# Optimization experiments

Measured on AMD Instinct MI355X. Metric: run time of the kernel, lower is better.

The kernel has to match this reference:

```python
import jax, jax.numpy as jnp
import numpy as np

B, T, N, E = 8, 32, 128, 2048
IN_DIM, HID, OUT = 512, 512, 512
SLOPE = 0.2  # GATConv default negative_slope


def setup_inputs() -> dict:
    key = jax.random.key(0)
    ks = jax.random.split(key, 12)
    x = jax.random.normal(ks[0], (B, T, N, IN_DIM), jnp.float32)
    edge_index = jax.random.randint(ks[1], (B, T, 2, E), 0, N)
    valid_step_index = jax.random.randint(ks[2], (B,), 1, T + 1)
    def lin(k, o, i):
        return jax.random.normal(k, (o, i), jnp.float32) / np.sqrt(i).astype(np.float32)
    W1 = lin(ks[3], HID, IN_DIM)
    a1_src = jax.random.normal(ks[4], (HID,), jnp.float32) / np.sqrt(HID).astype(np.float32)
    a1_dst = jax.random.normal(ks[5], (HID,), jnp.float32) / np.sqrt(HID).astype(np.float32)
    b1 = jnp.zeros((HID,), jnp.float32)
    W2 = lin(ks[6], OUT, HID)
    a2_src = jax.random.normal(ks[7], (OUT,), jnp.float32) / np.sqrt(OUT).astype(np.float32)
    a2_dst = jax.random.normal(ks[8], (OUT,), jnp.float32) / np.sqrt(OUT).astype(np.float32)
    b2 = jnp.zeros((OUT,), jnp.float32)
    W_time = jax.random.normal(ks[9], (T, T), jnp.float32) / np.sqrt(T).astype(np.float32)
    b_time = jnp.zeros((T,), jnp.float32)
    return dict(x=x, edge_index=edge_index, valid_step_index=valid_step_index,
                W1=W1, a1_src=a1_src, a1_dst=a1_dst, b1=b1,
                W2=W2, a2_src=a2_src, a2_dst=a2_dst, b2=b2,
                W_time=W_time, b_time=b_time)


def _gat(x, src, dst, W, a_src, a_dst, b):
    # Single-head PyG GATConv (concat=True, heads=1), self-loops already appended.
    n = x.shape[0]
    h = x @ W.T                                             # [N, H]
    e = jax.nn.leaky_relu((h @ a_src)[src] + (h @ a_dst)[dst], SLOPE)  # [E]
    m = jax.ops.segment_max(e, dst, num_segments=n)
    m = jnp.where(jnp.isfinite(m), m, 0.0)
    p = jnp.exp(e - m[dst])
    denom = jax.ops.segment_sum(p, dst, num_segments=n)
    alpha = p / denom[dst]                                  # segment softmax over incoming edges
    return jax.ops.segment_sum(h[src] * alpha[:, None], dst, num_segments=n) + b


def reference(x, edge_index, valid_step_index, W1, a1_src, a1_dst, b1,
              W2, a2_src, a2_dst, b2, W_time, b_time):
    b_, t_, n_, _ = x.shape
    g = b_ * t_
    xf = x.reshape(g, n_, -1)
    ei = edge_index.reshape(g, 2, -1)
    # add self loops (PyG GATConv default add_self_loops=True)
    loops = jnp.broadcast_to(jnp.arange(n_)[None, None, :], (g, 2, n_))
    ei = jnp.concatenate([ei, loops], axis=-1)
    src, dst = ei[:, 0], ei[:, 1]
    gat = jax.vmap(_gat, in_axes=(0, 0, 0, None, None, None, None))
    h = jax.nn.gelu(gat(xf, src, dst, W1, a1_src, a1_dst, b1), approximate=False)
    # F.dropout(p=0.2) is identity in eval mode
    h = gat(h, src, dst, W2, a2_src, a2_dst, b2)
    y = h.reshape(b_, t_, n_, -1)
    mask = (jnp.arange(t_)[None, :] < valid_step_index[:, None]).astype(y.dtype)
    y = y * mask[:, :, None, None]
    # TemporalConv: Conv2d(T, T, 1) over time-as-channel = linear mix across time, then GELU, residual
    fused = jax.nn.gelu(jnp.einsum('ts,bsnf->btnf', W_time, y)
                        + b_time[None, :, None, None], approximate=False)
    return fused + y
```

## Files before the change

kernel.cpp:

```cpp
#include <hip/hip_runtime.h>

using u16 = unsigned short;
using u32 = unsigned int;

typedef __bf16 bf16x8 __attribute__((ext_vector_type(8)));
typedef float  f32x4  __attribute__((ext_vector_type(4)));

__device__ __forceinline__ u16 f2bf(float f) {
    u32 u = __float_as_uint(f);
    u32 r = u + 0x7fffu + ((u >> 16) & 1u);
    return (u16)(r >> 16);
}
__device__ __forceinline__ float gelu_f(float x) {
    return 0.5f * x * (1.0f + erff(x * 0.70710678118654752440f));
}

#define GLOAD16(gp, lp) __builtin_amdgcn_global_load_lds( \
    (const __attribute__((address_space(1))) void*)(gp),  \
    (__attribute__((address_space(3))) void*)(lp), 16, 0, 0)
#define WAITV4  asm volatile("s_waitcnt vmcnt(4)" ::: "memory")
#define WAITV0  asm volatile("s_waitcnt vmcnt(0)" ::: "memory")
#define WAITL0  asm volatile("s_waitcnt lgkmcnt(0)" ::: "memory")

__global__ __launch_bounds__(256) void prep_kernel(
    const float* __restrict__ x, const float* __restrict__ W1, const float* __restrict__ W2,
    u16* __restrict__ Xb, u16* __restrict__ W1b, u16* __restrict__ W2b,
    float* __restrict__ Z)
{
    const int i0 = blockIdx.x * 256 + threadIdx.x;
    const int stride = gridDim.x * 256;
    if (i0 < 32768) ((float4*)Z)[i0] = make_float4(0.f, 0.f, 0.f, 0.f);
    for (int i = i0; i < 65536; i += stride) {
        float4 v = ((const float4*)W1)[i];
        ushort4 o; o.x = f2bf(v.x); o.y = f2bf(v.y); o.z = f2bf(v.z); o.w = f2bf(v.w);
        ((ushort4*)W1b)[i] = o;
    }
    for (int i = i0; i < 65536; i += stride) {
        float4 v = ((const float4*)W2)[i];
        ushort4 o; o.x = f2bf(v.x); o.y = f2bf(v.y); o.z = f2bf(v.z); o.w = f2bf(v.w);
        ((ushort4*)W2b)[i] = o;
    }
    for (int i = i0; i < 4194304; i += stride) {
        float4 v = ((const float4*)x)[i];
        ushort4 o; o.x = f2bf(v.x); o.y = f2bf(v.y); o.z = f2bf(v.z); o.w = f2bf(v.w);
        ((ushort4*)Xb)[i] = o;
    }
}

__global__ __launch_bounds__(256) void gat_gemm(
    const u16* __restrict__ A, const u16* __restrict__ Wb,
    const float* __restrict__ a_s, const float* __restrict__ a_d,
    u16* __restrict__ HT, float* __restrict__ SS, float* __restrict__ SD)
{
    __shared__ __align__(16) u16 As[2][128 * 32];
    __shared__ __align__(16) u16 Bs[2][128 * 32];
    __shared__ float sA[128], dA[128];

    const int tid  = threadIdx.x;
    const int lane = tid & 63;
    const int w    = tid >> 6;
    const int wm   = w & 1, wn = w >> 1;
    const int fr   = lane & 15;
    const int grp  = lane >> 4;
    const int bid  = (blockIdx.x & 7) * 128 + (blockIdx.x >> 3);
    const int g    = bid >> 2;
    const int tn   = (bid & 3) * 128;

    if (tid < 128) { sA[tid] = 0.f; dA[tid] = 0.f; }

    const int l3 = lane >> 3, l7 = lane & 7;
    const int cs = l7 ^ l3;
    const u16* Ag0 = A  + (size_t)g * 65536
                   + (size_t)(w * 32 + 2 * l3 + (cs >> 2)) * 512 + (cs & 3) * 8;
    const u16* Bg0 = Wb + (size_t)(tn + w * 32 + 2 * l3 + (cs >> 2)) * 512 + (cs & 3) * 8;

    const int sw = ((((fr & 1) << 2) | grp) ^ ((fr >> 1) & 7)) * 8;

    f32x4 acc[4][4] = {};

    GLOAD16(Ag0,                 &As[0][w * 1024]);
    GLOAD16(Ag0 + 16 * 512,      &As[0][w * 1024 + 512]);
    GLOAD16(Bg0,                 &Bs[0][w * 1024]);
    GLOAD16(Bg0 + 16 * 512,      &Bs[0][w * 1024 + 512]);
    GLOAD16(Ag0 + 32,            &As[1][w * 1024]);
    GLOAD16(Ag0 + 16 * 512 + 32, &As[1][w * 1024 + 512]);
    GLOAD16(Bg0 + 32,            &Bs[1][w * 1024]);
    GLOAD16(Bg0 + 16 * 512 + 32, &Bs[1][w * 1024 + 512]);

    for (int kt = 0; kt < 16; ++kt) {
        const int cur = kt & 1;
        if (kt < 15) { WAITV4; } else { WAITV0; }
        __builtin_amdgcn_s_barrier();
        bf16x8 af[4], bf[4];
        #pragma unroll
        for (int i = 0; i < 4; ++i) {
            af[i] = *(const bf16x8*)&As[cur][(wm * 32 + i * 8 + (fr >> 1)) * 64 + sw];
            bf[i] = *(const bf16x8*)&Bs[cur][(wn * 32 + i * 8 + (fr >> 1)) * 64 + sw];
        }
        WAITL0;
        __builtin_amdgcn_sched_barrier(0);
        __builtin_amdgcn_s_barrier();
        if (kt < 14) {
            GLOAD16(Ag0 + (kt + 2) * 32,            &As[cur][w * 1024]);
            GLOAD16(Ag0 + 16 * 512 + (kt + 2) * 32, &As[cur][w * 1024 + 512]);
            GLOAD16(Bg0 + (kt + 2) * 32,            &Bs[cur][w * 1024]);
            GLOAD16(Bg0 + 16 * 512 + (kt + 2) * 32, &Bs[cur][w * 1024 + 512]);
        }
        #pragma unroll
        for (int i = 0; i < 4; ++i)
            #pragma unroll
            for (int j = 0; j < 4; ++j)
                acc[i][j] = __builtin_amdgcn_mfma_f32_16x16x32_bf16(af[i], bf[j], acc[i][j], 0, 0, 0);
    }

    float asv[4], adv[4];
    #pragma unroll
    for (int j = 0; j < 4; ++j) {
        int f = tn + wn * 64 + j * 16 + fr;
        asv[j] = a_s[f]; adv[j] = a_d[f];
    }
    u16* Hg = HT + (size_t)g * 65536;
    #pragma unroll
    for (int i = 0; i < 4; ++i) {
        int node0 = wm * 64 + i * 16 + grp * 4;
        #pragma unroll
        for (int j = 0; j < 4; ++j) {
            int f = tn + wn * 64 + j * 16 + fr;
            ushort4 o;
            o.x = f2bf(acc[i][j][0]); o.y = f2bf(acc[i][j][1]);
            o.z = f2bf(acc[i][j][2]); o.w = f2bf(acc[i][j][3]);
            *(ushort4*)&Hg[(size_t)f * 128 + node0] = o;
        }
        #pragma unroll
        for (int r = 0; r < 4; ++r) {
            float s = acc[i][0][r] * asv[0] + acc[i][1][r] * asv[1]
                    + acc[i][2][r] * asv[2] + acc[i][3][r] * asv[3];
            float d = acc[i][0][r] * adv[0] + acc[i][1][r] * adv[1]
                    + acc[i][2][r] * adv[2] + acc[i][3][r] * adv[3];
            #pragma unroll
            for (int off = 1; off < 16; off <<= 1) {
                s += __shfl_xor(s, off);
                d += __shfl_xor(d, off);
            }
            if (fr == 0) {
                atomicAdd(&sA[node0 + r], s);
                atomicAdd(&dA[node0 + r], d);
            }
        }
    }
    __syncthreads();
    if (tid < 128) {
        atomicAdd(&SS[g * 128 + tid], sA[tid]);
        atomicAdd(&SD[g * 128 + tid], dA[tid]);
    }
}

template<int MODE>
__global__ __launch_bounds__(512) void gat_agg(
    const u16* __restrict__ HT, const int* __restrict__ ei,
    const float* __restrict__ SS, const float* __restrict__ SD,
    const float* __restrict__ bias, const int* __restrict__ valid,
    u16* __restrict__ outU, float* __restrict__ outF)
{
    __shared__ u16 Hts[32768];
    __shared__ u32 cntw[2048];
    __shared__ float stf[512];

    const int tid  = threadIdx.x;
    const int lane = tid & 63;
    const int w    = tid >> 6;
    const int rl   = lane & 15;
    const int grp  = lane >> 4;
    const int q    = blockIdx.x;
    const int g    = (q & 7) * 32 + (q >> 4);
    const int hf   = (q >> 3) & 1;
    const int bb   = g >> 5, tt = g & 31;

    const int4* es = (const int4*)(ei + (size_t)g * 4096);
    int4 e0 = es[tid], e1 = es[512 + tid];

    const u16* Hg = HT + (size_t)g * 65536 + (size_t)hf * 256 * 128;
    #pragma unroll
    for (int it = 0; it < 8; ++it) {
        int fl = it * 32 + (tid >> 4);
        int blk = tid & 15;
        GLOAD16(Hg + (size_t)fl * 128 + ((blk ^ (fl & 15)) * 8), &Hts[it * 4096 + w * 512]);
    }

    for (int i = tid; i < 2048; i += 512) cntw[i] = 0u;
    if (tid < 128) {
        stf[tid]       = SS[g * 128 + tid];
        stf[128 + tid] = SD[g * 128 + tid];
    }
    __syncthreads();

    atomicAdd(&cntw[e1.x * 16 + (e0.x >> 3)], 1u << ((e0.x & 7) * 4));
    atomicAdd(&cntw[e1.y * 16 + (e0.y >> 3)], 1u << ((e0.y & 7) * 4));
    atomicAdd(&cntw[e1.z * 16 + (e0.z >> 3)], 1u << ((e0.z & 7) * 4));
    atomicAdd(&cntw[e1.w * 16 + (e0.w >> 3)], 1u << ((e0.w & 7) * 4));
    if (tid < 128) atomicAdd(&cntw[tid * 16 + (tid >> 3)], 1u << ((tid & 7) * 4));
    __syncthreads();

    for (int r = 0; r < 16; ++r) {
        int m = w * 16 + r;
        float sdm = stf[128 + m];
        u32 w0 = cntw[m * 16 + (lane >> 3)];
        u32 w1 = cntw[m * 16 + 8 + (lane >> 3)];
        u32 c0 = (w0 >> ((lane & 7) * 4)) & 15u;
        u32 c1 = (w1 >> ((lane & 7) * 4)) & 15u;
        float E0 = stf[lane] + sdm;      E0 = E0 > 0.f ? E0 : 0.2f * E0;
        float E1 = stf[lane + 64] + sdm; E1 = E1 > 0.f ? E1 : 0.2f * E1;
        float mx = fmaxf(c0 ? E0 : -1e30f, c1 ? E1 : -1e30f);
        #pragma unroll
        for (int off = 1; off < 64; off <<= 1) mx = fmaxf(mx, __shfl_xor(mx, off));
        float p = (c0 ? (float)c0 * __expf(E0 - mx) : 0.f)
                + (c1 ? (float)c1 * __expf(E1 - mx) : 0.f);
        #pragma unroll
        for (int off = 1; off < 64; off <<= 1) p += __shfl_xor(p, off);
        if (lane == 0) { stf[256 + m] = mx; stf[384 + m] = 1.f / p; }
    }
    __syncthreads();

    const int m = w * 16 + rl;
    const float sdm = stf[128 + m], Mm = stf[256 + m], rDm = stf[384 + m];
    bf16x8 pa[4];
    #pragma unroll
    for (int kb = 0; kb < 4; ++kb) {
        u32 word = cntw[m * 16 + kb * 4 + grp];
        #pragma unroll
        for (int e = 0; e < 8; ++e) {
            u32 c = (word >> (e * 4)) & 15u;
            int s = kb * 32 + grp * 8 + e;
            float ev = stf[s] + sdm; ev = ev > 0.f ? ev : 0.2f * ev;
            float p = c ? (float)c * __expf(ev - Mm) * rDm : 0.f;
            pa[kb][e] = (__bf16)p;
        }
    }

    const float msk = (MODE == 1) ? ((tt < valid[bb]) ? 1.f : 0.f) : 1.f;
    #pragma unroll 1
    for (int jc = 0; jc < 4; ++jc) {
        f32x4 acc2[4] = {};
        __builtin_amdgcn_s_setprio(1);
        #pragma unroll
        for (int j4 = 0; j4 < 4; ++j4) {
            int fl = jc * 64 + j4 * 16 + rl;
            #pragma unroll
            for (int kb = 0; kb < 4; ++kb) {
                bf16x8 hb = *(const bf16x8*)&Hts[fl * 128 + (((kb * 4 + grp) ^ (fl & 15)) * 8)];
                acc2[j4] = __builtin_amdgcn_mfma_f32_16x16x32_bf16(pa[kb], hb, acc2[j4], 0, 0, 0);
            }
        }
        __builtin_amdgcn_s_setprio(0);
        #pragma unroll
        for (int j4 = 0; j4 < 4; ++j4) {
            int f = hf * 256 + jc * 64 + j4 * 16 + rl;
            float bv = bias[f];
            #pragma unroll
            for (int r = 0; r < 4; ++r) {
                int m2 = w * 16 + grp * 4 + r;
                if (MODE == 0)
                    outU[(size_t)g * 65536 + m2 * 512 + f] = f2bf(gelu_f(acc2[j4][r] + bv));
                else
                    outF[(size_t)g * 65536 + m2 * 512 + f] = (acc2[j4][r] + bv) * msk;
            }
        }
    }
}

__global__ __launch_bounds__(256) void timemix_kernel(float* __restrict__ y,
                                                      const float* __restrict__ Wt,
                                                      const float* __restrict__ bt) {
    __shared__ float wsm[1024];
    __shared__ float bts[32];
    int tid = threadIdx.x;
    for (int i = tid; i < 1024; i += 256) wsm[i] = Wt[i];
    if (tid < 32) bts[tid] = bt[tid];
    __syncthreads();
    int blk = blockIdx.x;
    int b = blk >> 8;
    int rem = blk & 255;
    int n = rem >> 1;
    int f = (rem & 1) * 256 + tid;
    size_t base = ((size_t)b * 4096 + n) * 512 + f;
    float ys[32];
    #pragma unroll
    for (int s = 0; s < 32; ++s) ys[s] = y[base + (size_t)s * 65536];
    #pragma unroll
    for (int t = 0; t < 32; ++t) {
        float a = bts[t];
        #pragma unroll
        for (int s = 0; s < 32; ++s) a += wsm[t * 32 + s] * ys[s];
        y[base + (size_t)t * 65536] = gelu_f(a) + ys[t];
    }
}

extern "C" void kernel_launch(void* const* d_in, const int* in_sizes, int n_in,
                              void* d_out, int out_size, void* d_ws, size_t ws_size,
                              hipStream_t stream) {
    const float* x     = (const float*)d_in[0];
    const int*   ei    = (const int*)d_in[1];
    const int*   valid = (const int*)d_in[2];
    const float* W1    = (const float*)d_in[3];
    const float* a1s   = (const float*)d_in[4];
    const float* a1d   = (const float*)d_in[5];
    const float* b1    = (const float*)d_in[6];
    const float* W2    = (const float*)d_in[7];
    const float* a2s   = (const float*)d_in[8];
    const float* a2d   = (const float*)d_in[9];
    const float* b2    = (const float*)d_in[10];
    const float* Wt    = (const float*)d_in[11];
    const float* bt    = (const float*)d_in[12];
    float* out = (float*)d_out;

    char* ws = (char*)d_ws;
    u16* Xb    = (u16*)(ws);
    u16* HTb   = (u16*)(ws + 33554432);
    u16* W1b   = (u16*)(ws + 67108864);
    u16* W2b   = (u16*)(ws + 67633152);
    float* SS1 = (float*)(ws + 68157440);
    float* SD1 = (float*)(ws + 68288512);
    float* SS2 = (float*)(ws + 68419584);
    float* SD2 = (float*)(ws + 68550656);

    prep_kernel<<<2048, 256, 0, stream>>>(x, W1, W2, Xb, W1b, W2b, SS1);

    gat_gemm<<<1024, 256, 0, stream>>>(Xb, W1b, a1s, a1d, HTb, SS1, SD1);
    gat_agg<0><<<512, 512, 0, stream>>>(HTb, ei, SS1, SD1, b1, nullptr, Xb, nullptr);

    gat_gemm<<<1024, 256, 0, stream>>>(Xb, W2b, a2s, a2d, HTb, SS2, SD2);
    gat_agg<1><<<512, 512, 0, stream>>>(HTb, ei, SS2, SD2, b2, valid, nullptr, out);

    timemix_kernel<<<2048, 256, 0, stream>>>(out, Wt, bt);
}
```

Before: 178.3 us.

## Fuse fp32-to-bf16 input conversion into first GAT GEMM A-tile loads

The first GEMM now reads fp32 x directly, converts it to bf16 in registers and writes the result to LDS with the swizzled layout. This removes the separate prep pass that wrote and reread a bf16 copy of x. The trade is a register-staged, single-barrier pipeline instead of the async global_load_lds double buffer. The aggregation kernel also swaps __syncthreads for explicit waitcnt plus s_barrier.

```diff
diff --git a/kernel.cpp b/kernel.cpp
--- a/kernel.cpp
+++ b/kernel.cpp
@@ -10,6 +10,9 @@
     u32 u = __float_as_uint(f);
     u32 r = u + 0x7fffu + ((u >> 16) & 1u);
     return (u16)(r >> 16);
+}
+__device__ __forceinline__ u32 pack2(float lo, float hi) {
+    return (u32)f2bf(lo) | ((u32)f2bf(hi) << 16);
 }
 __device__ __forceinline__ float gelu_f(float x) {
     return 0.5f * x * (1.0f + erff(x * 0.70710678118654752440f));
@@ -21,10 +24,11 @@
 #define WAITV4  asm volatile("s_waitcnt vmcnt(4)" ::: "memory")
 #define WAITV0  asm volatile("s_waitcnt vmcnt(0)" ::: "memory")
 #define WAITL0  asm volatile("s_waitcnt lgkmcnt(0)" ::: "memory")
+#define WAITVL0 asm volatile("s_waitcnt vmcnt(0) lgkmcnt(0)" ::: "memory")
 
 __global__ __launch_bounds__(256) void prep_kernel(
-    const float* __restrict__ x, const float* __restrict__ W1, const float* __restrict__ W2,
-    u16* __restrict__ Xb, u16* __restrict__ W1b, u16* __restrict__ W2b,
+    const float* __restrict__ W1, const float* __restrict__ W2,
+    u16* __restrict__ W1b, u16* __restrict__ W2b,
     float* __restrict__ Z)
 {
     const int i0 = blockIdx.x * 256 + threadIdx.x;
@@ -40,15 +44,11 @@
         ushort4 o; o.x = f2bf(v.x); o.y = f2bf(v.y); o.z = f2bf(v.z); o.w = f2bf(v.w);
         ((ushort4*)W2b)[i] = o;
     }
-    for (int i = i0; i < 4194304; i += stride) {
-        float4 v = ((const float4*)x)[i];
-        ushort4 o; o.x = f2bf(v.x); o.y = f2bf(v.y); o.z = f2bf(v.z); o.w = f2bf(v.w);
-        ((ushort4*)Xb)[i] = o;
-    }
-}
-
+}
+
+template<int AF32>
 __global__ __launch_bounds__(256) void gat_gemm(
-    const u16* __restrict__ A, const u16* __restrict__ Wb,
+    const void* __restrict__ Av, const u16* __restrict__ Wb,
     const float* __restrict__ a_s, const float* __restrict__ a_d,
     u16* __restrict__ HT, float* __restrict__ SS, float* __restrict__ SD)
 {
@@ -70,47 +70,111 @@
 
     const int l3 = lane >> 3, l7 = lane & 7;
     const int cs = l7 ^ l3;
-    const u16* Ag0 = A  + (size_t)g * 65536
-                   + (size_t)(w * 32 + 2 * l3 + (cs >> 2)) * 512 + (cs & 3) * 8;
     const u16* Bg0 = Wb + (size_t)(tn + w * 32 + 2 * l3 + (cs >> 2)) * 512 + (cs & 3) * 8;
 
     const int sw = ((((fr & 1) << 2) | grp) ^ ((fr >> 1) & 7)) * 8;
 
     f32x4 acc[4][4] = {};
 
-    GLOAD16(Ag0,                 &As[0][w * 1024]);
-    GLOAD16(Ag0 + 16 * 512,      &As[0][w * 1024 + 512]);
-    GLOAD16(Bg0,                 &Bs[0][w * 1024]);
-    GLOAD16(Bg0 + 16 * 512,      &Bs[0][w * 1024 + 512]);
-    GLOAD16(Ag0 + 32,            &As[1][w * 1024]);
-    GLOAD16(Ag0 + 16 * 512 + 32, &As[1][w * 1024 + 512]);
-    GLOAD16(Bg0 + 32,            &Bs[1][w * 1024]);
-    GLOAD16(Bg0 + 16 * 512 + 32, &Bs[1][w * 1024 + 512]);
-
-    for (int kt = 0; kt < 16; ++kt) {
-        const int cur = kt & 1;
-        if (kt < 15) { WAITV4; } else { WAITV0; }
-        __builtin_amdgcn_s_barrier();
-        bf16x8 af[4], bf[4];
-        #pragma unroll
-        for (int i = 0; i < 4; ++i) {
-            af[i] = *(const bf16x8*)&As[cur][(wm * 32 + i * 8 + (fr >> 1)) * 64 + sw];
-            bf[i] = *(const bf16x8*)&Bs[cur][(wn * 32 + i * 8 + (fr >> 1)) * 64 + sw];
-        }
-        WAITL0;
-        __builtin_amdgcn_sched_barrier(0);
-        __builtin_amdgcn_s_barrier();
-        if (kt < 14) {
-            GLOAD16(Ag0 + (kt + 2) * 32,            &As[cur][w * 1024]);
-            GLOAD16(Ag0 + 16 * 512 + (kt + 2) * 32, &As[cur][w * 1024 + 512]);
-            GLOAD16(Bg0 + (kt + 2) * 32,            &Bs[cur][w * 1024]);
-            GLOAD16(Bg0 + 16 * 512 + (kt + 2) * 32, &Bs[cur][w * 1024 + 512]);
-        }
-        #pragma unroll
-        for (int i = 0; i < 4; ++i)
-            #pragma unroll
-            for (int j = 0; j < 4; ++j)
-                acc[i][j] = __builtin_amdgcn_mfma_f32_16x16x32_bf16(af[i], bf[j], acc[i][j], 0, 0, 0);
+    if constexpr (AF32 == 0) {
+        const u16* Ag0 = (const u16*)Av + (size_t)g * 65536
+                       + (size_t)(w * 32 + 2 * l3 + (cs >> 2)) * 512 + (cs & 3) * 8;
+        GLOAD16(Ag0,                 &As[0][w * 1024]);
+        GLOAD16(Ag0 + 16 * 512,      &As[0][w * 1024 + 512]);
+        GLOAD16(Bg0,                 &Bs[0][w * 1024]);
+        GLOAD16(Bg0 + 16 * 512,      &Bs[0][w * 1024 + 512]);
+        GLOAD16(Ag0 + 32,            &As[1][w * 1024]);
+        GLOAD16(Ag0 + 16 * 512 + 32, &As[1][w * 1024 + 512]);
+        GLOAD16(Bg0 + 32,            &Bs[1][w * 1024]);
+        GLOAD16(Bg0 + 16 * 512 + 32, &Bs[1][w * 1024 + 512]);
+
+        for (int kt = 0; kt < 16; ++kt) {
+            const int cur = kt & 1;
+            if (kt < 15) { WAITV4; } else { WAITV0; }
+            __builtin_amdgcn_s_barrier();
+            bf16x8 af[4], bf[4];
+            #pragma unroll
+            for (int i = 0; i < 4; ++i) {
+                af[i] = *(const bf16x8*)&As[cur][(wm * 32 + i * 8 + (fr >> 1)) * 64 + sw];
+                bf[i] = *(const bf16x8*)&Bs[cur][(wn * 32 + i * 8 + (fr >> 1)) * 64 + sw];
+            }
+            WAITL0;
+            __builtin_amdgcn_sched_barrier(0);
+            __builtin_amdgcn_s_barrier();
+            if (kt < 14) {
+                GLOAD16(Ag0 + (kt + 2) * 32,            &As[cur][w * 1024]);
+                GLOAD16(Ag0 + 16 * 512 + (kt + 2) * 32, &As[cur][w * 1024 + 512]);
+                GLOAD16(Bg0 + (kt + 2) * 32,            &Bs[cur][w * 1024]);
+                GLOAD16(Bg0 + 16 * 512 + (kt + 2) * 32, &Bs[cur][w * 1024 + 512]);
+            }
+            #pragma unroll
+            for (int i = 0; i < 4; ++i)
+                #pragma unroll
+                for (int j = 0; j < 4; ++j)
+                    acc[i][j] = __builtin_amdgcn_mfma_f32_16x16x32_bf16(af[i], bf[j], acc[i][j], 0, 0, 0);
+        }
+    } else {
+        const float* xg = (const float*)Av + (size_t)g * 65536;
+        const int R  = tid >> 1;
+        const int cb = (tid & 1) * 2;
+        const float* xrow = xg + (size_t)R * 512 + cb * 8;
+        const int P  = R >> 1;
+        const int b0 = (((R & 1) << 2) | cb) ^ (P & 7);
+        const int b1 = (((R & 1) << 2) | (cb + 1)) ^ (P & 7);
+        const int wa0 = P * 64 + b0 * 8;
+        const int wa1 = P * 64 + b1 * 8;
+
+        {
+            f32x4 xa = *(const f32x4*)(xrow + 0);
+            f32x4 xb = *(const f32x4*)(xrow + 4);
+            f32x4 xc = *(const f32x4*)(xrow + 8);
+            f32x4 xd = *(const f32x4*)(xrow + 12);
+            uint4 q0, q1;
+            q0.x = pack2(xa[0], xa[1]); q0.y = pack2(xa[2], xa[3]);
+            q0.z = pack2(xb[0], xb[1]); q0.w = pack2(xb[2], xb[3]);
+            q1.x = pack2(xc[0], xc[1]); q1.y = pack2(xc[2], xc[3]);
+            q1.z = pack2(xd[0], xd[1]); q1.w = pack2(xd[2], xd[3]);
+            *(uint4*)&As[0][wa0] = q0;
+            *(uint4*)&As[0][wa1] = q1;
+            GLOAD16(Bg0,            &Bs[0][w * 1024]);
+            GLOAD16(Bg0 + 16 * 512, &Bs[0][w * 1024 + 512]);
+        }
+        __syncthreads();
+
+        for (int kt = 0; kt < 16; ++kt) {
+            const int cur = kt & 1, nb = cur ^ 1;
+            f32x4 xa, xb, xc, xd;
+            if (kt < 15) {
+                const float* xr = xrow + (kt + 1) * 32;
+                xa = *(const f32x4*)(xr + 0);
+                xb = *(const f32x4*)(xr + 4);
+                xc = *(const f32x4*)(xr + 8);
+                xd = *(const f32x4*)(xr + 12);
+                GLOAD16(Bg0 + (kt + 1) * 32,            &Bs[nb][w * 1024]);
+                GLOAD16(Bg0 + 16 * 512 + (kt + 1) * 32, &Bs[nb][w * 1024 + 512]);
+            }
+            bf16x8 af[4], bf[4];
+            #pragma unroll
+            for (int i = 0; i < 4; ++i) {
+                af[i] = *(const bf16x8*)&As[cur][(wm * 32 + i * 8 + (fr >> 1)) * 64 + sw];
+                bf[i] = *(const bf16x8*)&Bs[cur][(wn * 32 + i * 8 + (fr >> 1)) * 64 + sw];
+            }
+            #pragma unroll
+            for (int i = 0; i < 4; ++i)
+                #pragma unroll
+                for (int j = 0; j < 4; ++j)
+                    acc[i][j] = __builtin_amdgcn_mfma_f32_16x16x32_bf16(af[i], bf[j], acc[i][j], 0, 0, 0);
+            if (kt < 15) {
+                uint4 q0, q1;
+                q0.x = pack2(xa[0], xa[1]); q0.y = pack2(xa[2], xa[3]);
+                q0.z = pack2(xb[0], xb[1]); q0.w = pack2(xb[2], xb[3]);
+                q1.x = pack2(xc[0], xc[1]); q1.y = pack2(xc[2], xc[3]);
+                q1.z = pack2(xd[0], xd[1]); q1.w = pack2(xd[2], xd[3]);
+                *(uint4*)&As[nb][wa0] = q0;
+                *(uint4*)&As[nb][wa1] = q1;
+            }
+            __syncthreads();
+        }
     }
 
     float asv[4], adv[4];
@@ -192,14 +256,16 @@
         stf[tid]       = SS[g * 128 + tid];
         stf[128 + tid] = SD[g * 128 + tid];
     }
-    __syncthreads();
+    WAITL0;
+    __builtin_amdgcn_s_barrier();
 
     atomicAdd(&cntw[e1.x * 16 + (e0.x >> 3)], 1u << ((e0.x & 7) * 4));
     atomicAdd(&cntw[e1.y * 16 + (e0.y >> 3)], 1u << ((e0.y & 7) * 4));
     atomicAdd(&cntw[e1.z * 16 + (e0.z >> 3)], 1u << ((e0.z & 7) * 4));
     atomicAdd(&cntw[e1.w * 16 + (e0.w >> 3)], 1u << ((e0.w & 7) * 4));
     if (tid < 128) atomicAdd(&cntw[tid * 16 + (tid >> 3)], 1u << ((tid & 7) * 4));
-    __syncthreads();
+    WAITL0;
+    __builtin_amdgcn_s_barrier();
 
     for (int r = 0; r < 16; ++r) {
         int m = w * 16 + r;
@@ -219,7 +285,8 @@
         for (int off = 1; off < 64; off <<= 1) p += __shfl_xor(p, off);
         if (lane == 0) { stf[256 + m] = mx; stf[384 + m] = 1.f / p; }
     }
-    __syncthreads();
+    WAITVL0;
+    __builtin_amdgcn_s_barrier();
 
     const int m = w * 16 + rl;
     const float sdm = stf[128 + m], Mm = stf[256 + m], rDm = stf[384 + m];
@@ -323,12 +390,12 @@
     float* SS2 = (float*)(ws + 68419584);
     float* SD2 = (float*)(ws + 68550656);
 
-    prep_kernel<<<2048, 256, 0, stream>>>(x, W1, W2, Xb, W1b, W2b, SS1);
-
-    gat_gemm<<<1024, 256, 0, stream>>>(Xb, W1b, a1s, a1d, HTb, SS1, SD1);
+    prep_kernel<<<512, 256, 0, stream>>>(W1, W2, W1b, W2b, SS1);
+
+    gat_gemm<1><<<1024, 256, 0, stream>>>(x, W1b, a1s, a1d, HTb, SS1, SD1);
     gat_agg<0><<<512, 512, 0, stream>>>(HTb, ei, SS1, SD1, b1, nullptr, Xb, nullptr);
 
-    gat_gemm<<<1024, 256, 0, stream>>>(Xb, W2b, a2s, a2d, HTb, SS2, SD2);
+    gat_gemm<0><<<1024, 256, 0, stream>>>(Xb, W2b, a2s, a2d, HTb, SS2, SD2);
     gat_agg<1><<<512, 512, 0, stream>>>(HTb, ei, SS2, SD2, b2, valid, nullptr, out);
 
     timemix_kernel<<<2048, 256, 0, stream>>>(out, Wt, bt);
```

Result: slower. 182.0 us (+2.1%).

## Load GEMM weight fragments directly to registers and stage aggregation barriers

Applied to the files above, without the earlier changes.

In the GAT projection GEMM, the weight (B) operand is no longer staged through LDS. Each wave loads its bf16 weight fragments straight from global memory into double-buffered registers, and the vmcnt waits are adjusted to match. The aggregation kernel prefetches the per-node attention scalars into registers, replaces __syncthreads with lgkmcnt waits plus raw barriers, and waits on the H-tile LDS loads chunk by chunk so MFMA work can start before all of H has arrived. This trades LDS traffic and occupancy for more VGPRs and redundant global weight reads across waves, and the vmcnt counting is fragile.

```diff
diff --git a/kernel.cpp b/kernel.cpp
--- a/kernel.cpp
+++ b/kernel.cpp
@@ -18,7 +18,10 @@
 #define GLOAD16(gp, lp) __builtin_amdgcn_global_load_lds( \
     (const __attribute__((address_space(1))) void*)(gp),  \
     (__attribute__((address_space(3))) void*)(lp), 16, 0, 0)
+#define WAITV10 asm volatile("s_waitcnt vmcnt(10)" ::: "memory")
+#define WAITV6  asm volatile("s_waitcnt vmcnt(6)" ::: "memory")
 #define WAITV4  asm volatile("s_waitcnt vmcnt(4)" ::: "memory")
+#define WAITV2  asm volatile("s_waitcnt vmcnt(2)" ::: "memory")
 #define WAITV0  asm volatile("s_waitcnt vmcnt(0)" ::: "memory")
 #define WAITL0  asm volatile("s_waitcnt lgkmcnt(0)" ::: "memory")
 
@@ -53,7 +56,6 @@
     u16* __restrict__ HT, float* __restrict__ SS, float* __restrict__ SD)
 {
     __shared__ __align__(16) u16 As[2][128 * 32];
-    __shared__ __align__(16) u16 Bs[2][128 * 32];
     __shared__ float sA[128], dA[128];
 
     const int tid  = threadIdx.x;
@@ -70,9 +72,10 @@
 
     const int l3 = lane >> 3, l7 = lane & 7;
     const int cs = l7 ^ l3;
-    const u16* Ag0 = A  + (size_t)g * 65536
+    const u16* Ag0 = A + (size_t)g * 65536
                    + (size_t)(w * 32 + 2 * l3 + (cs >> 2)) * 512 + (cs & 3) * 8;
-    const u16* Bg0 = Wb + (size_t)(tn + w * 32 + 2 * l3 + (cs >> 2)) * 512 + (cs & 3) * 8;
+
+    const u16* wg = Wb + (size_t)(tn + wn * 64 + fr) * 512 + grp * 8;
 
     const int sw = ((((fr & 1) << 2) | grp) ^ ((fr >> 1) & 7)) * 8;
 
@@ -80,37 +83,53 @@
 
     GLOAD16(Ag0,                 &As[0][w * 1024]);
     GLOAD16(Ag0 + 16 * 512,      &As[0][w * 1024 + 512]);
-    GLOAD16(Bg0,                 &Bs[0][w * 1024]);
-    GLOAD16(Bg0 + 16 * 512,      &Bs[0][w * 1024 + 512]);
     GLOAD16(Ag0 + 32,            &As[1][w * 1024]);
     GLOAD16(Ag0 + 16 * 512 + 32, &As[1][w * 1024 + 512]);
-    GLOAD16(Bg0 + 32,            &Bs[1][w * 1024]);
-    GLOAD16(Bg0 + 16 * 512 + 32, &Bs[1][w * 1024 + 512]);
-
+    bf16x8 wA[4], wB[4];
+    #pragma unroll
+    for (int j = 0; j < 4; ++j) wA[j] = *(const bf16x8*)&wg[j * 16 * 512];
+    #pragma unroll
+    for (int j = 0; j < 4; ++j) wB[j] = *(const bf16x8*)&wg[j * 16 * 512 + 32];
+
+    #pragma unroll 2
     for (int kt = 0; kt < 16; ++kt) {
         const int cur = kt & 1;
-        if (kt < 15) { WAITV4; } else { WAITV0; }
+        if (kt < 15) { WAITV10; } else { WAITV4; }
         __builtin_amdgcn_s_barrier();
-        bf16x8 af[4], bf[4];
-        #pragma unroll
-        for (int i = 0; i < 4; ++i) {
+        bf16x8 af[4];
+        #pragma unroll
+        for (int i = 0; i < 4; ++i)
             af[i] = *(const bf16x8*)&As[cur][(wm * 32 + i * 8 + (fr >> 1)) * 64 + sw];
-            bf[i] = *(const bf16x8*)&Bs[cur][(wn * 32 + i * 8 + (fr >> 1)) * 64 + sw];
-        }
         WAITL0;
         __builtin_amdgcn_sched_barrier(0);
         __builtin_amdgcn_s_barrier();
         if (kt < 14) {
             GLOAD16(Ag0 + (kt + 2) * 32,            &As[cur][w * 1024]);
             GLOAD16(Ag0 + 16 * 512 + (kt + 2) * 32, &As[cur][w * 1024 + 512]);
-            GLOAD16(Bg0 + (kt + 2) * 32,            &Bs[cur][w * 1024]);
-            GLOAD16(Bg0 + 16 * 512 + (kt + 2) * 32, &Bs[cur][w * 1024 + 512]);
-        }
-        #pragma unroll
-        for (int i = 0; i < 4; ++i)
-            #pragma unroll
-            for (int j = 0; j < 4; ++j)
-                acc[i][j] = __builtin_amdgcn_mfma_f32_16x16x32_bf16(af[i], bf[j], acc[i][j], 0, 0, 0);
+        }
+        if (cur == 0) {
+            #pragma unroll
+            for (int i = 0; i < 4; ++i)
+                #pragma unroll
+                for (int j = 0; j < 4; ++j)
+                    acc[i][j] = __builtin_amdgcn_mfma_f32_16x16x32_bf16(af[i], wA[j], acc[i][j], 0, 0, 0);
+            if (kt < 14) {
+                #pragma unroll
+                for (int j = 0; j < 4; ++j)
+                    wA[j] = *(const bf16x8*)&wg[j * 16 * 512 + (kt + 2) * 32];
+            }
+        } else {
+            #pragma unroll
+            for (int i = 0; i < 4; ++i)
+                #pragma unroll
+                for (int j = 0; j < 4; ++j)
+                    acc[i][j] = __builtin_amdgcn_mfma_f32_16x16x32_bf16(af[i], wB[j], acc[i][j], 0, 0, 0);
+            if (kt < 14) {
+                #pragma unroll
+                for (int j = 0; j < 4; ++j)
+                    wB[j] = *(const bf16x8*)&wg[j * 16 * 512 + (kt + 2) * 32];
+            }
+        }
     }
 
     float asv[4], adv[4];
@@ -178,6 +197,8 @@
 
     const int4* es = (const int4*)(ei + (size_t)g * 4096);
     int4 e0 = es[tid], e1 = es[512 + tid];
+    float s0 = 0.f, s1 = 0.f;
+    if (tid < 128) { s0 = SS[g * 128 + tid]; s1 = SD[g * 128 + tid]; }
 
     const u16* Hg = HT + (size_t)g * 65536 + (size_t)hf * 256 * 128;
     #pragma unroll
@@ -188,18 +209,17 @@
     }
 
     for (int i = tid; i < 2048; i += 512) cntw[i] = 0u;
-    if (tid < 128) {
-        stf[tid]       = SS[g * 128 + tid];
-        stf[128 + tid] = SD[g * 128 + tid];
-    }
-    __syncthreads();
+    if (tid < 128) { stf[tid] = s0; stf[128 + tid] = s1; }
+    WAITL0;
+    __builtin_amdgcn_s_barrier();
 
     atomicAdd(&cntw[e1.x * 16 + (e0.x >> 3)], 1u << ((e0.x & 7) * 4));
     atomicAdd(&cntw[e1.y * 16 + (e0.y >> 3)], 1u << ((e0.y & 7) * 4));
     atomicAdd(&cntw[e1.z * 16 + (e0.z >> 3)], 1u << ((e0.z & 7) * 4));
     atomicAdd(&cntw[e1.w * 16 + (e0.w >> 3)], 1u << ((e0.w & 7) * 4));
     if (tid < 128) atomicAdd(&cntw[tid * 16 + (tid >> 3)], 1u << ((tid & 7) * 4));
-    __syncthreads();
+    WAITL0;
+    __builtin_amdgcn_s_barrier();
 
     for (int r = 0; r < 16; ++r) {
         int m = w * 16 + r;
@@ -219,7 +239,8 @@
         for (int off = 1; off < 64; off <<= 1) p += __shfl_xor(p, off);
         if (lane == 0) { stf[256 + m] = mx; stf[384 + m] = 1.f / p; }
     }
-    __syncthreads();
+    WAITL0;
+    __builtin_amdgcn_s_barrier();
 
     const int m = w * 16 + rl;
     const float sdm = stf[128 + m], Mm = stf[256 + m], rDm = stf[384 + m];
@@ -240,6 +261,11 @@
     const float msk = (MODE == 1) ? ((tt < valid[bb]) ? 1.f : 0.f) : 1.f;
     #pragma unroll 1
     for (int jc = 0; jc < 4; ++jc) {
+        if      (jc == 0) { WAITV6; }
+        else if (jc == 1) { WAITV4; }
+        else if (jc == 2) { WAITV2; }
+        else              { WAITV0; }
+        __builtin_amdgcn_s_barrier();
         f32x4 acc2[4] = {};
         __builtin_amdgcn_s_setprio(1);
         #pragma unroll
```

New measurement: 207.4 us. 16.3% more time.
